# Kernel optimization log

Hardware: AMD Instinct MI355X
Metric: run time of the kernel (lower is better)

Reference implementation:

```python
import jax, jax.numpy as jnp
import numpy as np

B, D_IN, H1, H2, LAT, K = 32768, 512, 256, 128, 64, 2048
BN_EPS = 1e-5
COMMIT = 0.25


def _linear_w(k, i, o):
    # xavier-uniform-ish init
    lim = np.sqrt(6.0 / (i + o)).astype(np.float32)
    return jax.random.uniform(k, (i, o), jnp.float32, -lim, lim)


def _bn_params(keys, n):
    g = jax.random.uniform(keys[0], (n,), jnp.float32, 0.5, 1.5)
    b = 0.1 * jax.random.normal(keys[1], (n,), jnp.float32)
    m = 0.1 * jax.random.normal(keys[2], (n,), jnp.float32)
    v = jax.random.uniform(keys[3], (n,), jnp.float32, 0.5, 1.5)
    return g, b, m, v


def setup_inputs() -> dict:
    key = jax.random.key(0)
    ks = jax.random.split(key, 32)
    inp = {"x": jax.random.normal(ks[0], (B, D_IN), jnp.float32)}
    # encoder: 512 -> 256 -> 128 -> 64
    inp["ew1"], inp["eb1"] = _linear_w(ks[1], D_IN, H1), jnp.zeros((H1,), jnp.float32)
    inp["eg1"], inp["ebt1"], inp["em1"], inp["ev1"] = _bn_params(jax.random.split(ks[2], 4), H1)
    inp["ew2"], inp["eb2"] = _linear_w(ks[3], H1, H2), jnp.zeros((H2,), jnp.float32)
    inp["eg2"], inp["ebt2"], inp["em2"], inp["ev2"] = _bn_params(jax.random.split(ks[4], 4), H2)
    inp["ew3"], inp["eb3"] = _linear_w(ks[5], H2, LAT), jnp.zeros((LAT,), jnp.float32)
    # codebook (num_embeddings, latent_dim)
    inp["codebook"] = _linear_w(ks[6], K, LAT).reshape(K, LAT)
    # decoder: 64 -> 128 -> 256 -> 512
    inp["dw1"], inp["db1"] = _linear_w(ks[7], LAT, H2), jnp.zeros((H2,), jnp.float32)
    inp["dg1"], inp["dbt1"], inp["dm1"], inp["dv1"] = _bn_params(jax.random.split(ks[8], 4), H2)
    inp["dw2"], inp["db2"] = _linear_w(ks[9], H2, H1), jnp.zeros((H1,), jnp.float32)
    inp["dg2"], inp["dbt2"], inp["dm2"], inp["dv2"] = _bn_params(jax.random.split(ks[10], 4), H1)
    inp["dw3"], inp["db3"] = _linear_w(ks[11], H1, D_IN), jnp.zeros((D_IN,), jnp.float32)
    return inp


def _bn(x, g, b, m, v):
    # BatchNorm1d in eval mode: running stats
    return (x - m) * (g * jax.lax.rsqrt(v + BN_EPS)) + b


def reference(x, ew1, eb1, eg1, ebt1, em1, ev1,
              ew2, eb2, eg2, ebt2, em2, ev2,
              ew3, eb3, codebook,
              dw1, db1, dg1, dbt1, dm1, dv1,
              dw2, db2, dg2, dbt2, dm2, dv2,
              dw3, db3):
    # ---- encoder MLP (Dropout is identity in eval) ----
    h = _bn(jax.nn.relu(x @ ew1 + eb1), eg1, ebt1, em1, ev1)
    h = _bn(jax.nn.relu(h @ ew2 + eb2), eg2, ebt2, em2, ev2)
    z_e = h @ ew3 + eb3  # [B, LAT]

    # ---- vector quantization: cdist + argmin + gather ----
    # squared L2 distance (argmin-equivalent to cdist p=2)
    d2 = (jnp.sum(z_e * z_e, axis=1, keepdims=True)
          + jnp.sum(codebook * codebook, axis=1)[None, :]
          - 2.0 * (z_e @ codebook.T))  # [B, K]
    idx = jnp.argmin(d2, axis=-1)  # [B]
    z_q = codebook[idx]  # gather, [B, LAT]

    codebook_loss = jnp.mean((z_q - jax.lax.stop_gradient(z_e)) ** 2)
    commit_loss = jnp.mean((z_e - jax.lax.stop_gradient(z_q)) ** 2)
    vq_loss = codebook_loss + COMMIT * commit_loss

    # straight-through estimator
    z_q = z_e + jax.lax.stop_gradient(z_q - z_e)

    # ---- decoder MLP ----
    h = _bn(jax.nn.relu(z_q @ dw1 + db1), dg1, dbt1, dm1, dv1)
    h = _bn(jax.nn.relu(h @ dw2 + db2), dg2, dbt2, dm2, dv2)
    x_recon = h @ dw3 + db3  # [B, D_IN]

    recon_err = jnp.mean((x_recon - x) ** 2)
    return x_recon, vq_loss, idx, recon_err
```

## Files before the change

kernel.cpp:

```cpp
#include <hip/hip_runtime.h>

#define B_ROWS 32768
#define D_IN   512
#define H1_N   256
#define H2_N   128
#define LAT_N  64
#define K_CB   2048

#define BM 64
#define BN 128
#define BK 32

#define VQ_MARGIN 4.0e-3f

typedef __attribute__((ext_vector_type(8))) short s8v;
typedef __attribute__((ext_vector_type(4))) float f4v;

__device__ inline unsigned short f2bf(float f) {
    union { float f; unsigned u; } v; v.f = f;
    unsigned r = v.u + 0x7fffu + ((v.u >> 16) & 1u);
    return (unsigned short)(r >> 16);
}
__device__ inline float bf2f(unsigned short h) {
    union { unsigned u; float f; } v; v.u = ((unsigned)h) << 16;
    return v.f;
}

#define SWZ(row) ((((row) >> 2) & 7) << 3)

template <int MODE>
__global__ __launch_bounds__(256, 4) void gemm_fused(
    const float* __restrict__ A, const float* __restrict__ W,
    const float* __restrict__ bias,
    const float* __restrict__ bn_g, const float* __restrict__ bn_b,
    const float* __restrict__ bn_m, const float* __restrict__ bn_v,
    float* __restrict__ out, int M, int N)
{
    __shared__ float sA[BK][BM];
    __shared__ float sB[BK][BN];
    const int tid = threadIdx.x;
    const int tr = tid >> 4;
    const int tc = tid & 15;
    const int row0 = blockIdx.x * BM;
    const int n0   = blockIdx.y * BN;

    float acc[4][8];
#pragma unroll
    for (int i = 0; i < 4; ++i)
#pragma unroll
        for (int j = 0; j < 8; ++j) acc[i][j] = 0.f;

    for (int k0 = 0; k0 < M; k0 += BK) {
#pragma unroll
        for (int it = 0; it < 2; ++it) {
            int s = tid + it * 256;
            int m = s >> 3;
            int kq = s & 7;
            float4 v = *reinterpret_cast<const float4*>(
                &A[(size_t)(row0 + m) * M + k0 + kq * 4]);
            int kk = kq * 4;
            sA[kk + 0][m ^ SWZ(kk + 0)] = v.x;
            sA[kk + 1][m ^ SWZ(kk + 1)] = v.y;
            sA[kk + 2][m ^ SWZ(kk + 2)] = v.z;
            sA[kk + 3][m ^ SWZ(kk + 3)] = v.w;
        }
#pragma unroll
        for (int it = 0; it < 4; ++it) {
            int s = tid + it * 256;
            int k = s >> 5;
            int nq = s & 31;
            int n = n0 + nq * 4;
            float4 v = make_float4(0.f, 0.f, 0.f, 0.f);
            if (n < N)
                v = *reinterpret_cast<const float4*>(&W[(size_t)(k0 + k) * N + n]);
            *reinterpret_cast<float4*>(&sB[k][nq * 4]) = v;
        }
        __syncthreads();
#pragma unroll 4
        for (int k = 0; k < BK; ++k) {
            int ac = (tr * 4) ^ SWZ(k);
            float4 a0 = *reinterpret_cast<float4*>(&sA[k][ac]);
            float4 b0 = *reinterpret_cast<float4*>(&sB[k][tc * 8]);
            float4 b1 = *reinterpret_cast<float4*>(&sB[k][tc * 8 + 4]);
            float a[4] = {a0.x, a0.y, a0.z, a0.w};
            float b[8] = {b0.x, b0.y, b0.z, b0.w, b1.x, b1.y, b1.z, b1.w};
#pragma unroll
            for (int i = 0; i < 4; ++i)
#pragma unroll
                for (int j = 0; j < 8; ++j)
                    acc[i][j] = fmaf(a[i], b[j], acc[i][j]);
        }
        __syncthreads();
    }

    const int nb = n0 + tc * 8;
    if (nb < N) {
        float bi[8], sc[8], sh[8];
#pragma unroll
        for (int j = 0; j < 8; ++j) {
            int n = nb + j;
            bi[j] = bias[n];
            if (MODE == 0) {
                float s = bn_g[n] * rsqrtf(bn_v[n] + 1e-5f);
                sc[j] = s;
                sh[j] = bn_b[n] - bn_m[n] * s;
            }
        }
#pragma unroll
        for (int i = 0; i < 4; ++i) {
            int row = row0 + tr * 4 + i;
            float o[8];
#pragma unroll
            for (int j = 0; j < 8; ++j) {
                float v = acc[i][j] + bi[j];
                if (MODE == 0) {
                    v = v > 0.f ? v : 0.f;
                    v = v * sc[j] + sh[j];
                }
                o[j] = v;
            }
            *reinterpret_cast<float4*>(&out[(size_t)row * N + nb]) =
                make_float4(o[0], o[1], o[2], o[3]);
            *reinterpret_cast<float4*>(&out[(size_t)row * N + nb + 4]) =
                make_float4(o[4], o[5], o[6], o[7]);
        }
    }
}

__global__ __launch_bounds__(256) void wprep(
    const float* __restrict__ w, unsigned short* __restrict__ w_hi,
    unsigned short* __restrict__ w_lo, int K, int N)
{
    int idx = blockIdx.x * 256 + threadIdx.x;
    if (idx >= N * K) return;
    int n = idx / K, k = idx - n * K;
    float f = w[(size_t)k * N + n];
    unsigned u = __float_as_uint(f);
    float lo = f - __uint_as_float(u & 0xffff0000u);
    w_hi[idx] = (unsigned short)(u >> 16);
    w_lo[idx] = (unsigned short)(__float_as_uint(lo) >> 16);
}

template <int MODE, int K>
__global__ __launch_bounds__(256, 2) void mfma_gemm(
    const float* __restrict__ A,
    const unsigned short* __restrict__ w_hi,
    const unsigned short* __restrict__ w_lo,
    const float* __restrict__ bias,
    const float* __restrict__ bn_g, const float* __restrict__ bn_b,
    const float* __restrict__ bn_m, const float* __restrict__ bn_v,
    float* __restrict__ out,
    const float* __restrict__ xref, float* __restrict__ partials, int N)
{
    const int lane = threadIdx.x & 63;
    const int wv = threadIdx.x >> 6;
    const int wr = wv >> 1, wc = wv & 1;
    const int rbase = blockIdx.x * 128 + wr * 64;
    const int cbase = blockIdx.y * 128 + wc * 64;
    const int lr = lane & 15, lg = lane >> 4;

    f4v acc[4][4];
#pragma unroll
    for (int rt = 0; rt < 4; ++rt)
#pragma unroll
        for (int ct = 0; ct < 4; ++ct)
            acc[rt][ct] = (f4v){0.f, 0.f, 0.f, 0.f};

#pragma unroll
    for (int ks = 0; ks < K / 32; ++ks) {
        s8v ah[4], al[4], bh[4], bl[4];
#pragma unroll
        for (int rt = 0; rt < 4; ++rt) {
            const float* p =
                &A[(size_t)(rbase + rt * 16 + lr) * K + ks * 32 + lg * 8];
            float4 v0 = *reinterpret_cast<const float4*>(p);
            float4 v1 = *reinterpret_cast<const float4*>(p + 4);
            float fv[8] = {v0.x, v0.y, v0.z, v0.w, v1.x, v1.y, v1.z, v1.w};
            unsigned uu[8], ll[8];
#pragma unroll
            for (int j = 0; j < 8; ++j) {
                uu[j] = __float_as_uint(fv[j]);
                float lo = fv[j] - __uint_as_float(uu[j] & 0xffff0000u);
                ll[j] = __float_as_uint(lo);
            }
            union { s8v v; unsigned w[4]; } H, L;
#pragma unroll
            for (int m = 0; m < 4; ++m) {
                H.w[m] = __builtin_amdgcn_perm(uu[2 * m + 1], uu[2 * m], 0x07060302u);
                L.w[m] = __builtin_amdgcn_perm(ll[2 * m + 1], ll[2 * m], 0x07060302u);
            }
            ah[rt] = H.v;
            al[rt] = L.v;
        }
#pragma unroll
        for (int ct = 0; ct < 4; ++ct) {
            size_t off = (size_t)(cbase + ct * 16 + lr) * K + ks * 32 + lg * 8;
            bh[ct] = *reinterpret_cast<const s8v*>(&w_hi[off]);
            bl[ct] = *reinterpret_cast<const s8v*>(&w_lo[off]);
        }
#pragma unroll
        for (int rt = 0; rt < 4; ++rt)
#pragma unroll
            for (int ct = 0; ct < 4; ++ct) {
                acc[rt][ct] = __builtin_amdgcn_mfma_f32_16x16x32_bf16(
                    ah[rt], bh[ct], acc[rt][ct], 0, 0, 0);
                acc[rt][ct] = __builtin_amdgcn_mfma_f32_16x16x32_bf16(
                    al[rt], bh[ct], acc[rt][ct], 0, 0, 0);
                acc[rt][ct] = __builtin_amdgcn_mfma_f32_16x16x32_bf16(
                    ah[rt], bl[ct], acc[rt][ct], 0, 0, 0);
            }
    }

    float sq = 0.f;
#pragma unroll
    for (int ct = 0; ct < 4; ++ct) {
        int col = cbase + ct * 16 + lr;
        float bi = bias[col];
        float sc = 0.f, sh = 0.f;
        if (MODE == 0) {
            float s = bn_g[col] * rsqrtf(bn_v[col] + 1e-5f);
            sc = s;
            sh = bn_b[col] - bn_m[col] * s;
        }
#pragma unroll
        for (int rt = 0; rt < 4; ++rt)
#pragma unroll
            for (int i = 0; i < 4; ++i) {
                int row = rbase + rt * 16 + lg * 4 + i;
                float v = acc[rt][ct][i] + bi;
                if (MODE == 0) v = fmaxf(v, 0.f) * sc + sh;
                if (MODE == 2) {
                    float d = v - xref[(size_t)row * N + col];
                    sq = fmaf(d, d, sq);
                }
                out[(size_t)row * N + col] = v;
            }
    }
    if (MODE == 2) {
        __shared__ float red[256];
        red[threadIdx.x] = sq;
        __syncthreads();
        for (int off = 128; off > 0; off >>= 1) {
            if (threadIdx.x < off) red[threadIdx.x] += red[threadIdx.x + off];
            __syncthreads();
        }
        if (threadIdx.x == 0)
            partials[blockIdx.y * gridDim.x + blockIdx.x] = red[0];
    }
}

__global__ __launch_bounds__(256) void vq_prep(
    const float* __restrict__ cb, unsigned short* __restrict__ cb_hi,
    unsigned short* __restrict__ cb_lo, float* __restrict__ cn,
    int* __restrict__ rcnt)
{
    if (blockIdx.x == 0 && threadIdx.x == 0) rcnt[0] = 0;
    int j = blockIdx.x * 256 + threadIdx.x;
    float s = 0.f;
#pragma unroll
    for (int lq = 0; lq < 16; ++lq) {
        float4 v = *reinterpret_cast<const float4*>(&cb[(size_t)j * LAT_N + lq * 4]);
        float e[4] = {v.x, v.y, v.z, v.w};
        ushort4 h, l;
        unsigned short* hp = &h.x;
        unsigned short* lp = &l.x;
#pragma unroll
        for (int t = 0; t < 4; ++t) {
            s = fmaf(e[t], e[t], s);
            unsigned short hb = f2bf(e[t]);
            hp[t] = hb;
            lp[t] = f2bf(e[t] - bf2f(hb));
        }
        *reinterpret_cast<ushort4*>(&cb_hi[(size_t)j * LAT_N + lq * 4]) = h;
        *reinterpret_cast<ushort4*>(&cb_lo[(size_t)j * LAT_N + lq * 4]) = l;
    }
    cn[j] = s;
}

__global__ __launch_bounds__(256) void vq_mfma(
    const float* __restrict__ z, const unsigned short* __restrict__ cb_hi,
    const unsigned short* __restrict__ cb_lo, const float* __restrict__ cnorm,
    float4* __restrict__ cand)
{
    const int lane = threadIdx.x & 63;
    const int wid  = blockIdx.x * 4 + (threadIdx.x >> 6);
    const int rbase = (wid >> 3) * 64;
    const int cblk  = wid & 7;
    const int cbase = cblk * 256;
    const int lr = lane & 15;
    const int lg = lane >> 4;

    s8v a_hi[4][2], a_lo[4][2];
#pragma unroll
    for (int rt = 0; rt < 4; ++rt) {
        int row = rbase + rt * 16 + lr;
#pragma unroll
        for (int ks = 0; ks < 2; ++ks) {
            const float* p = &z[(size_t)row * LAT_N + ks * 32 + lg * 8];
            float4 v0 = *reinterpret_cast<const float4*>(p);
            float4 v1 = *reinterpret_cast<const float4*>(p + 4);
            float vv[8] = {v0.x, v0.y, v0.z, v0.w, v1.x, v1.y, v1.z, v1.w};
#pragma unroll
            for (int jj = 0; jj < 8; ++jj) {
                unsigned short hb = f2bf(vv[jj]);
                a_hi[rt][ks][jj] = (short)hb;
                a_lo[rt][ks][jj] = (short)f2bf(vv[jj] - bf2f(hb));
            }
        }
    }

    float b1[4][4], b2[4][4];
    int j1[4][4];
#pragma unroll
    for (int rt = 0; rt < 4; ++rt)
#pragma unroll
        for (int i = 0; i < 4; ++i) {
            b1[rt][i] = 3.4e38f; b2[rt][i] = 3.4e38f; j1[rt][i] = 0;
        }

    for (int ct = 0; ct < 16; ++ct) {
        int col = cbase + ct * 16 + lr;
        const unsigned short* ph = &cb_hi[(size_t)col * LAT_N + lg * 8];
        const unsigned short* pl = &cb_lo[(size_t)col * LAT_N + lg * 8];
        s8v bh0 = *reinterpret_cast<const s8v*>(ph);
        s8v bh1 = *reinterpret_cast<const s8v*>(ph + 32);
        s8v bl0 = *reinterpret_cast<const s8v*>(pl);
        s8v bl1 = *reinterpret_cast<const s8v*>(pl + 32);
        float cn = cnorm[col];
#pragma unroll
        for (int rt = 0; rt < 4; ++rt) {
            f4v acc = {0.f, 0.f, 0.f, 0.f};
            acc = __builtin_amdgcn_mfma_f32_16x16x32_bf16(a_hi[rt][0], bh0, acc, 0, 0, 0);
            acc = __builtin_amdgcn_mfma_f32_16x16x32_bf16(a_hi[rt][1], bh1, acc, 0, 0, 0);
            acc = __builtin_amdgcn_mfma_f32_16x16x32_bf16(a_lo[rt][0], bh0, acc, 0, 0, 0);
            acc = __builtin_amdgcn_mfma_f32_16x16x32_bf16(a_lo[rt][1], bh1, acc, 0, 0, 0);
            acc = __builtin_amdgcn_mfma_f32_16x16x32_bf16(a_hi[rt][0], bl0, acc, 0, 0, 0);
            acc = __builtin_amdgcn_mfma_f32_16x16x32_bf16(a_hi[rt][1], bl1, acc, 0, 0, 0);
#pragma unroll
            for (int i = 0; i < 4; ++i) {
                float d = fmaf(-2.f, acc[i], cn);
                if (d < b1[rt][i]) {
                    b2[rt][i] = b1[rt][i];
                    b1[rt][i] = d;
                    j1[rt][i] = col;
                } else if (d < b2[rt][i]) {
                    b2[rt][i] = d;
                }
            }
        }
    }

#pragma unroll
    for (int off = 1; off < 16; off <<= 1) {
#pragma unroll
        for (int rt = 0; rt < 4; ++rt)
#pragma unroll
            for (int i = 0; i < 4; ++i) {
                float o1 = __shfl_xor(b1[rt][i], off);
                float o2 = __shfl_xor(b2[rt][i], off);
                int oj = __shfl_xor(j1[rt][i], off);
                float nb2 = fminf(fmaxf(b1[rt][i], o1), fminf(b2[rt][i], o2));
                if (o1 < b1[rt][i] ||
                    (o1 == b1[rt][i] && oj < j1[rt][i])) {
                    b1[rt][i] = o1;
                    j1[rt][i] = oj;
                }
                b2[rt][i] = nb2;
            }
    }
    if (lr == 0) {
#pragma unroll
        for (int rt = 0; rt < 4; ++rt)
#pragma unroll
            for (int i = 0; i < 4; ++i) {
                int row = rbase + rt * 16 + lg * 4 + i;
                cand[(size_t)row * 8 + cblk] = make_float4(
                    b1[rt][i], __int_as_float(j1[rt][i]), b2[rt][i], 0.f);
            }
    }
}

__global__ __launch_bounds__(256) void vq_merge(
    const float4* __restrict__ cand, float* __restrict__ idxf,
    int* __restrict__ rlist, int* __restrict__ rcnt)
{
    int row = blockIdx.x * 256 + threadIdx.x;
    const float4* c = &cand[(size_t)row * 8];
    float4 c0 = c[0];
    float b1 = c0.x, b2 = c0.z;
    int j1 = __float_as_int(c0.y);
#pragma unroll
    for (int t = 1; t < 8; ++t) {
        float4 ct = c[t];
        float o1 = ct.x, o2 = ct.z;
        int oj = __float_as_int(ct.y);
        float nb2 = fminf(fmaxf(b1, o1), fminf(b2, o2));
        if (o1 < b1 || (o1 == b1 && oj < j1)) { b1 = o1; j1 = oj; }
        b2 = nb2;
    }
    idxf[row] = (float)j1;
    if (!(b2 - b1 >= VQ_MARGIN)) {
        int s = atomicAdd(rcnt, 1);
        if (s < B_ROWS) rlist[s] = row;
    }
}

#define RB 8
__global__ __launch_bounds__(256) void vq_repair(
    const int* __restrict__ rcnt, const int* __restrict__ rlist,
    const float* __restrict__ z, const float* __restrict__ cb,
    const float* __restrict__ cn, float* __restrict__ idxf)
{
    __shared__ float sz[RB][LAT_N];
    __shared__ float rv[256];
    __shared__ int ri[256];
    const int tid = threadIdx.x;
    const int count = min(rcnt[0], B_ROWS);
    if (blockIdx.x * RB >= count) return;
    for (int base = blockIdx.x * RB; base < count; base += gridDim.x * RB) {
        int nr = min(RB, count - base);
        __syncthreads();
        for (int s = tid; s < nr * LAT_N; s += 256) {
            int r = s >> 6, d = s & 63;
            int rr = rlist[base + r];
            rr = ((unsigned)rr < (unsigned)B_ROWS) ? rr : 0;
            sz[r][d] = z[(size_t)rr * LAT_N + d];
        }
        __syncthreads();
        float bv[RB];
        int bj[RB];
#pragma unroll
        for (int r = 0; r < RB; ++r) { bv[r] = 3.4e38f; bj[r] = 0; }
        for (int k = 0; k < K_CB / 256; ++k) {
            int cidx = tid + k * 256;
            float acc[RB];
#pragma unroll
            for (int r = 0; r < RB; ++r) acc[r] = 0.f;
            const float* cp = &cb[(size_t)cidx * LAT_N];
#pragma unroll 2
            for (int d4 = 0; d4 < 16; ++d4) {
                float4 cv = *reinterpret_cast<const float4*>(cp + d4 * 4);
#pragma unroll
                for (int r = 0; r < RB; ++r) {
                    acc[r] = fmaf(sz[r][d4 * 4 + 0], cv.x, acc[r]);
                    acc[r] = fmaf(sz[r][d4 * 4 + 1], cv.y, acc[r]);
                    acc[r] = fmaf(sz[r][d4 * 4 + 2], cv.z, acc[r]);
                    acc[r] = fmaf(sz[r][d4 * 4 + 3], cv.w, acc[r]);
                }
            }
            float cnv = cn[cidx];
#pragma unroll
            for (int r = 0; r < RB; ++r) {
                float d = fmaf(-2.f, acc[r], cnv);
                if (d < bv[r] || (d == bv[r] && cidx < bj[r])) {
                    bv[r] = d; bj[r] = cidx;
                }
            }
        }
        for (int r = 0; r < RB; ++r) {
            if (r >= nr) break;
            rv[tid] = bv[r];
            ri[tid] = bj[r];
            __syncthreads();
            for (int off = 128; off > 0; off >>= 1) {
                if (tid < off) {
                    float ov = rv[tid + off];
                    int oi = ri[tid + off];
                    if (ov < rv[tid] || (ov == rv[tid] && oi < ri[tid])) {
                        rv[tid] = ov; ri[tid] = oi;
                    }
                }
                __syncthreads();
            }
            if (tid == 0) {
                int rr = rlist[base + r];
                if ((unsigned)rr < (unsigned)B_ROWS)
                    idxf[rr] = (float)ri[0];
            }
            __syncthreads();
        }
    }
}

__global__ __launch_bounds__(256) void vq_zqloss(
    const float* __restrict__ idxf, const float* __restrict__ z,
    const float* __restrict__ cb, float* __restrict__ zq,
    float* __restrict__ partials)
{
    __shared__ float red[256];
    int tid = threadIdx.x;
    int row = blockIdx.x * 256 + tid;
    int bj = (int)idxf[row];
    bj = ((unsigned)bj < (unsigned)K_CB) ? bj : 0;
    float sq = 0.f;
#pragma unroll
    for (int lq = 0; lq < 16; ++lq) {
        float4 cv = *reinterpret_cast<const float4*>(&cb[(size_t)bj * LAT_N + lq * 4]);
        float4 zv = *reinterpret_cast<const float4*>(&z[(size_t)row * LAT_N + lq * 4]);
        *reinterpret_cast<float4*>(&zq[(size_t)row * LAT_N + lq * 4]) = cv;
        float d0 = cv.x - zv.x, d1 = cv.y - zv.y;
        float d2 = cv.z - zv.z, d3 = cv.w - zv.w;
        sq = fmaf(d0, d0, sq); sq = fmaf(d1, d1, sq);
        sq = fmaf(d2, d2, sq); sq = fmaf(d3, d3, sq);
    }
    red[tid] = sq;
    __syncthreads();
    for (int off = 128; off > 0; off >>= 1) {
        if (tid < off) red[tid] += red[tid + off];
        __syncthreads();
    }
    if (tid == 0) partials[blockIdx.x] = red[0];
}

__global__ __launch_bounds__(256) void finalize_kernel(
    const float* __restrict__ vqp, int nvq,
    const float* __restrict__ rep, int nre,
    float* __restrict__ vq_out, float* __restrict__ re_out)
{
    __shared__ float s[256];
    int tid = threadIdx.x;
    float a = 0.f;
    for (int i = tid; i < nvq; i += 256) a += vqp[i];
    s[tid] = a;
    __syncthreads();
    for (int off = 128; off > 0; off >>= 1) {
        if (tid < off) s[tid] += s[tid + off];
        __syncthreads();
    }
    if (tid == 0) *vq_out = 1.25f * s[0] / (float)(B_ROWS * LAT_N);
    __syncthreads();
    float b = 0.f;
    for (int i = tid; i < nre; i += 256) b += rep[i];
    s[tid] = b;
    __syncthreads();
    for (int off = 128; off > 0; off >>= 1) {
        if (tid < off) s[tid] += s[tid + off];
        __syncthreads();
    }
    if (tid == 0) *re_out = s[0] / (float)(B_ROWS * D_IN);
}

extern "C" void kernel_launch(void* const* d_in, const int* in_sizes, int n_in,
                              void* d_out, int out_size, void* d_ws, size_t ws_size,
                              hipStream_t stream)
{
    const float* x    = (const float*)d_in[0];
    const float* ew1  = (const float*)d_in[1];
    const float* eb1  = (const float*)d_in[2];
    const float* eg1  = (const float*)d_in[3];
    const float* ebt1 = (const float*)d_in[4];
    const float* em1  = (const float*)d_in[5];
    const float* ev1  = (const float*)d_in[6];
    const float* ew2  = (const float*)d_in[7];
    const float* eb2  = (const float*)d_in[8];
    const float* eg2  = (const float*)d_in[9];
    const float* ebt2 = (const float*)d_in[10];
    const float* em2  = (const float*)d_in[11];
    const float* ev2  = (const float*)d_in[12];
    const float* ew3  = (const float*)d_in[13];
    const float* eb3  = (const float*)d_in[14];
    const float* cb   = (const float*)d_in[15];
    const float* dw1  = (const float*)d_in[16];
    const float* db1  = (const float*)d_in[17];
    const float* dg1  = (const float*)d_in[18];
    const float* dbt1 = (const float*)d_in[19];
    const float* dm1  = (const float*)d_in[20];
    const float* dv1  = (const float*)d_in[21];
    const float* dw2  = (const float*)d_in[22];
    const float* db2  = (const float*)d_in[23];
    const float* dg2  = (const float*)d_in[24];
    const float* dbt2 = (const float*)d_in[25];
    const float* dm2  = (const float*)d_in[26];
    const float* dv2  = (const float*)d_in[27];
    const float* dw3  = (const float*)d_in[28];
    const float* db3  = (const float*)d_in[29];

    float* outf = (float*)d_out;
    const size_t XR_OFF = 0;
    const size_t VQ_OFF = (size_t)B_ROWS * D_IN;
    const size_t IDX_OFF = VQ_OFF + 1;
    const size_t RE_OFF = IDX_OFF + B_ROWS;

    float* wsf = (float*)d_ws;
    size_t off = 0;
    float* buf256 = wsf + off; off += (size_t)B_ROWS * H1_N;
    float* buf128 = wsf + off; off += (size_t)B_ROWS * H2_N;
    float* zbuf   = wsf + off; off += (size_t)B_ROWS * LAT_N;
    float* zqbuf  = wsf + off; off += (size_t)B_ROWS * LAT_N;
    float* cnbuf  = wsf + off; off += K_CB;
    float* vqp    = wsf + off; off += 128;
    float* rep    = wsf + off; off += 1024;
    unsigned short* cbhi = (unsigned short*)(wsf + off); off += K_CB * LAT_N / 2;
    unsigned short* cblo = (unsigned short*)(wsf + off); off += K_CB * LAT_N / 2;
    float4* candb = (float4*)(wsf + off); off += (size_t)B_ROWS * 8 * 4;
    int* rcnt  = (int*)(wsf + off); off += 16;
    int* rlist = (int*)(wsf + off); off += B_ROWS;
    unsigned short* w1hi = (unsigned short*)(wsf + off); off += (H2_N * LAT_N) / 2;
    unsigned short* w1lo = (unsigned short*)(wsf + off); off += (H2_N * LAT_N) / 2;
    unsigned short* w2hi = (unsigned short*)(wsf + off); off += (H1_N * H2_N) / 2;
    unsigned short* w2lo = (unsigned short*)(wsf + off); off += (H1_N * H2_N) / 2;
    unsigned short* w3hi = (unsigned short*)(wsf + off); off += (D_IN * H1_N) / 2;
    unsigned short* w3lo = (unsigned short*)(wsf + off); off += (D_IN * H1_N) / 2;

    dim3 blk(256);
    const int GX = B_ROWS / BM;
    const int GXM = B_ROWS / 128;

    vq_prep<<<dim3(K_CB / 256), blk, 0, stream>>>(cb, cbhi, cblo, cnbuf, rcnt);
    wprep<<<dim3((LAT_N * H2_N + 255) / 256), blk, 0, stream>>>(dw1, w1hi, w1lo, LAT_N, H2_N);
    wprep<<<dim3((H2_N * H1_N + 255) / 256), blk, 0, stream>>>(dw2, w2hi, w2lo, H2_N, H1_N);
    wprep<<<dim3((H1_N * D_IN + 255) / 256), blk, 0, stream>>>(dw3, w3hi, w3lo, H1_N, D_IN);

    gemm_fused<0><<<dim3(GX, H1_N / BN), blk, 0, stream>>>(
        x, ew1, eb1, eg1, ebt1, em1, ev1, buf256, D_IN, H1_N);
    gemm_fused<0><<<dim3(GX, 1), blk, 0, stream>>>(
        buf256, ew2, eb2, eg2, ebt2, em2, ev2, buf128, H1_N, H2_N);
    gemm_fused<1><<<dim3(GX, 1), blk, 0, stream>>>(
        buf128, ew3, eb3, nullptr, nullptr, nullptr, nullptr, zbuf, H2_N, LAT_N);

    vq_mfma<<<dim3(1024), blk, 0, stream>>>(zbuf, cbhi, cblo, cnbuf, candb);
    vq_merge<<<dim3(B_ROWS / 256), blk, 0, stream>>>(
        candb, outf + IDX_OFF, rlist, rcnt);
    vq_repair<<<dim3(256), blk, 0, stream>>>(
        rcnt, rlist, zbuf, cb, cnbuf, outf + IDX_OFF);
    vq_zqloss<<<dim3(B_ROWS / 256), blk, 0, stream>>>(
        outf + IDX_OFF, zbuf, cb, zqbuf, vqp);

    mfma_gemm<0, LAT_N><<<dim3(GXM, H2_N / 128), blk, 0, stream>>>(
        zqbuf, w1hi, w1lo, db1, dg1, dbt1, dm1, dv1, buf128, nullptr, nullptr, H2_N);
    mfma_gemm<0, H2_N><<<dim3(GXM, H1_N / 128), blk, 0, stream>>>(
        buf128, w2hi, w2lo, db2, dg2, dbt2, dm2, dv2, buf256, nullptr, nullptr, H1_N);
    mfma_gemm<2, H1_N><<<dim3(GXM, D_IN / 128), blk, 0, stream>>>(
        buf256, w3hi, w3lo, db3, nullptr, nullptr, nullptr, nullptr,
        outf + XR_OFF, x, rep, D_IN);

    finalize_kernel<<<dim3(1), blk, 0, stream>>>(
        vqp, 128, rep, 1024, outf + VQ_OFF, outf + RE_OFF);
}
```

Baseline: 417.9 us.

## Store decoder activations as split bf16 hi/lo and retile encoder GEMMs

Decoder MFMA GEMMs now read activations already split into bf16 hi/lo planes, written by the previous layer's epilogue and by vq_zqloss (which copies the pre-split codebook rows). This removes the per-load fp32-to-bf16 split work in the GEMM inner loop while keeping the same number of bytes per activation. The encoder SIMT GEMM gains a 128-row tile variant for the first layer, with changed column mapping and occupancy hints. The lo part now uses round-to-nearest, which slightly changes the numerics. The epilogue issues scalar 16-bit stores to two planes, which may coalesce poorly.

```diff
diff --git a/kernel.cpp b/kernel.cpp
--- a/kernel.cpp
+++ b/kernel.cpp
@@ -7,7 +7,6 @@
 #define LAT_N  64
 #define K_CB   2048
 
-#define BM 64
 #define BN 128
 #define BK 32
 
@@ -28,31 +27,32 @@
 
 #define SWZ(row) ((((row) >> 2) & 7) << 3)
 
-template <int MODE>
-__global__ __launch_bounds__(256, 4) void gemm_fused(
+template <int MODE, int BMT>
+__global__ __launch_bounds__(256, (BMT == 128) ? 2 : 6) void gemm_fused(
     const float* __restrict__ A, const float* __restrict__ W,
     const float* __restrict__ bias,
     const float* __restrict__ bn_g, const float* __restrict__ bn_b,
     const float* __restrict__ bn_m, const float* __restrict__ bn_v,
     float* __restrict__ out, int M, int N)
 {
-    __shared__ float sA[BK][BM];
+    constexpr int MR = BMT / 16;
+    __shared__ float sA[BK][BMT];
     __shared__ float sB[BK][BN];
     const int tid = threadIdx.x;
     const int tr = tid >> 4;
     const int tc = tid & 15;
-    const int row0 = blockIdx.x * BM;
+    const int row0 = blockIdx.x * BMT;
     const int n0   = blockIdx.y * BN;
 
-    float acc[4][8];
-#pragma unroll
-    for (int i = 0; i < 4; ++i)
+    float acc[MR][8];
+#pragma unroll
+    for (int i = 0; i < MR; ++i)
 #pragma unroll
         for (int j = 0; j < 8; ++j) acc[i][j] = 0.f;
 
     for (int k0 = 0; k0 < M; k0 += BK) {
 #pragma unroll
-        for (int it = 0; it < 2; ++it) {
+        for (int it = 0; it < BMT / 32; ++it) {
             int s = tid + it * 256;
             int m = s >> 3;
             int kq = s & 7;
@@ -78,14 +78,21 @@
         __syncthreads();
 #pragma unroll 4
         for (int k = 0; k < BK; ++k) {
-            int ac = (tr * 4) ^ SWZ(k);
-            float4 a0 = *reinterpret_cast<float4*>(&sA[k][ac]);
-            float4 b0 = *reinterpret_cast<float4*>(&sB[k][tc * 8]);
-            float4 b1 = *reinterpret_cast<float4*>(&sB[k][tc * 8 + 4]);
-            float a[4] = {a0.x, a0.y, a0.z, a0.w};
+            int ac = (tr * MR) ^ SWZ(k);
+            float a[MR];
+            {
+                float4 a0 = *reinterpret_cast<float4*>(&sA[k][ac]);
+                a[0] = a0.x; a[1] = a0.y; a[2] = a0.z; a[3] = a0.w;
+                if constexpr (MR == 8) {
+                    float4 a1 = *reinterpret_cast<float4*>(&sA[k][ac + 4]);
+                    a[4] = a1.x; a[5] = a1.y; a[6] = a1.z; a[7] = a1.w;
+                }
+            }
+            float4 b0 = *reinterpret_cast<float4*>(&sB[k][tc * 4]);
+            float4 b1 = *reinterpret_cast<float4*>(&sB[k][64 + tc * 4]);
             float b[8] = {b0.x, b0.y, b0.z, b0.w, b1.x, b1.y, b1.z, b1.w};
 #pragma unroll
-            for (int i = 0; i < 4; ++i)
+            for (int i = 0; i < MR; ++i)
 #pragma unroll
                 for (int j = 0; j < 8; ++j)
                     acc[i][j] = fmaf(a[i], b[j], acc[i][j]);
@@ -93,36 +100,45 @@
         __syncthreads();
     }
 
-    const int nb = n0 + tc * 8;
-    if (nb < N) {
-        float bi[8], sc[8], sh[8];
-#pragma unroll
-        for (int j = 0; j < 8; ++j) {
-            int n = nb + j;
-            bi[j] = bias[n];
-            if (MODE == 0) {
-                float s = bn_g[n] * rsqrtf(bn_v[n] + 1e-5f);
-                sc[j] = s;
-                sh[j] = bn_b[n] - bn_m[n] * s;
-            }
-        }
-#pragma unroll
-        for (int i = 0; i < 4; ++i) {
-            int row = row0 + tr * 4 + i;
-            float o[8];
-#pragma unroll
-            for (int j = 0; j < 8; ++j) {
-                float v = acc[i][j] + bi[j];
+    const int nb0 = n0 + tc * 4;
+    const int nb1 = n0 + 64 + tc * 4;
+    float bi[8], sc[8], sh[8];
+#pragma unroll
+    for (int g = 0; g < 2; ++g) {
+        int nb = g ? nb1 : nb0;
+        if (nb < N) {
+#pragma unroll
+            for (int j = 0; j < 4; ++j) {
+                int n = nb + j;
+                bi[g * 4 + j] = bias[n];
                 if (MODE == 0) {
-                    v = v > 0.f ? v : 0.f;
-                    v = v * sc[j] + sh[j];
-                }
-                o[j] = v;
-            }
-            *reinterpret_cast<float4*>(&out[(size_t)row * N + nb]) =
-                make_float4(o[0], o[1], o[2], o[3]);
-            *reinterpret_cast<float4*>(&out[(size_t)row * N + nb + 4]) =
-                make_float4(o[4], o[5], o[6], o[7]);
+                    float s = bn_g[n] * rsqrtf(bn_v[n] + 1e-5f);
+                    sc[g * 4 + j] = s;
+                    sh[g * 4 + j] = bn_b[n] - bn_m[n] * s;
+                }
+            }
+        }
+    }
+#pragma unroll
+    for (int i = 0; i < MR; ++i) {
+        int row = row0 + tr * MR + i;
+#pragma unroll
+        for (int g = 0; g < 2; ++g) {
+            int nb = g ? nb1 : nb0;
+            if (nb < N) {
+                float o[4];
+#pragma unroll
+                for (int j = 0; j < 4; ++j) {
+                    float v = acc[i][g * 4 + j] + bi[g * 4 + j];
+                    if (MODE == 0) {
+                        v = v > 0.f ? v : 0.f;
+                        v = v * sc[g * 4 + j] + sh[g * 4 + j];
+                    }
+                    o[j] = v;
+                }
+                *reinterpret_cast<float4*>(&out[(size_t)row * N + nb]) =
+                    make_float4(o[0], o[1], o[2], o[3]);
+            }
         }
     }
 }
@@ -138,18 +154,20 @@
     unsigned u = __float_as_uint(f);
     float lo = f - __uint_as_float(u & 0xffff0000u);
     w_hi[idx] = (unsigned short)(u >> 16);
-    w_lo[idx] = (unsigned short)(__float_as_uint(lo) >> 16);
+    w_lo[idx] = f2bf(lo);
 }
 
 template <int MODE, int K>
 __global__ __launch_bounds__(256, 2) void mfma_gemm(
-    const float* __restrict__ A,
+    const unsigned short* __restrict__ A_hi,
+    const unsigned short* __restrict__ A_lo,
     const unsigned short* __restrict__ w_hi,
     const unsigned short* __restrict__ w_lo,
     const float* __restrict__ bias,
     const float* __restrict__ bn_g, const float* __restrict__ bn_b,
     const float* __restrict__ bn_m, const float* __restrict__ bn_v,
-    float* __restrict__ out,
+    unsigned short* __restrict__ out_hi, unsigned short* __restrict__ out_lo,
+    float* __restrict__ out_f32,
     const float* __restrict__ xref, float* __restrict__ partials, int N)
 {
     const int lane = threadIdx.x & 63;
@@ -171,26 +189,9 @@
         s8v ah[4], al[4], bh[4], bl[4];
 #pragma unroll
         for (int rt = 0; rt < 4; ++rt) {
-            const float* p =
-                &A[(size_t)(rbase + rt * 16 + lr) * K + ks * 32 + lg * 8];
-            float4 v0 = *reinterpret_cast<const float4*>(p);
-            float4 v1 = *reinterpret_cast<const float4*>(p + 4);
-            float fv[8] = {v0.x, v0.y, v0.z, v0.w, v1.x, v1.y, v1.z, v1.w};
-            unsigned uu[8], ll[8];
-#pragma unroll
-            for (int j = 0; j < 8; ++j) {
-                uu[j] = __float_as_uint(fv[j]);
-                float lo = fv[j] - __uint_as_float(uu[j] & 0xffff0000u);
-                ll[j] = __float_as_uint(lo);
-            }
-            union { s8v v; unsigned w[4]; } H, L;
-#pragma unroll
-            for (int m = 0; m < 4; ++m) {
-                H.w[m] = __builtin_amdgcn_perm(uu[2 * m + 1], uu[2 * m], 0x07060302u);
-                L.w[m] = __builtin_amdgcn_perm(ll[2 * m + 1], ll[2 * m], 0x07060302u);
-            }
-            ah[rt] = H.v;
-            al[rt] = L.v;
+            size_t off = (size_t)(rbase + rt * 16 + lr) * K + ks * 32 + lg * 8;
+            ah[rt] = *reinterpret_cast<const s8v*>(&A_hi[off]);
+            al[rt] = *reinterpret_cast<const s8v*>(&A_lo[off]);
         }
 #pragma unroll
         for (int ct = 0; ct < 4; ++ct) {
@@ -228,12 +229,18 @@
             for (int i = 0; i < 4; ++i) {
                 int row = rbase + rt * 16 + lg * 4 + i;
                 float v = acc[rt][ct][i] + bi;
-                if (MODE == 0) v = fmaxf(v, 0.f) * sc + sh;
+                if (MODE == 0) {
+                    v = fmaxf(v, 0.f) * sc + sh;
+                    unsigned u = __float_as_uint(v);
+                    out_hi[(size_t)row * N + col] = (unsigned short)(u >> 16);
+                    out_lo[(size_t)row * N + col] =
+                        f2bf(v - __uint_as_float(u & 0xffff0000u));
+                }
                 if (MODE == 2) {
                     float d = v - xref[(size_t)row * N + col];
                     sq = fmaf(d, d, sq);
-                }
-                out[(size_t)row * N + col] = v;
+                    out_f32[(size_t)row * N + col] = v;
+                }
             }
     }
     if (MODE == 2) {
@@ -484,7 +491,10 @@
 
 __global__ __launch_bounds__(256) void vq_zqloss(
     const float* __restrict__ idxf, const float* __restrict__ z,
-    const float* __restrict__ cb, float* __restrict__ zq,
+    const float* __restrict__ cb,
+    const unsigned short* __restrict__ cbhi,
+    const unsigned short* __restrict__ cblo,
+    unsigned short* __restrict__ zqhi, unsigned short* __restrict__ zqlo,
     float* __restrict__ partials)
 {
     __shared__ float red[256];
@@ -497,12 +507,18 @@
     for (int lq = 0; lq < 16; ++lq) {
         float4 cv = *reinterpret_cast<const float4*>(&cb[(size_t)bj * LAT_N + lq * 4]);
         float4 zv = *reinterpret_cast<const float4*>(&z[(size_t)row * LAT_N + lq * 4]);
-        *reinterpret_cast<float4*>(&zq[(size_t)row * LAT_N + lq * 4]) = cv;
         float d0 = cv.x - zv.x, d1 = cv.y - zv.y;
         float d2 = cv.z - zv.z, d3 = cv.w - zv.w;
         sq = fmaf(d0, d0, sq); sq = fmaf(d1, d1, sq);
         sq = fmaf(d2, d2, sq); sq = fmaf(d3, d3, sq);
     }
+    const uint4* gh = reinterpret_cast<const uint4*>(&cbhi[(size_t)bj * LAT_N]);
+    const uint4* gl = reinterpret_cast<const uint4*>(&cblo[(size_t)bj * LAT_N]);
+    uint4* dh = reinterpret_cast<uint4*>(&zqhi[(size_t)row * LAT_N]);
+    uint4* dl = reinterpret_cast<uint4*>(&zqlo[(size_t)row * LAT_N]);
+#pragma unroll
+    for (int q = 0; q < 8; ++q) { dh[q] = gh[q]; dl[q] = gl[q]; }
+
     red[tid] = sq;
     __syncthreads();
     for (int off = 128; off > 0; off >>= 1) {
@@ -586,7 +602,6 @@
     float* buf256 = wsf + off; off += (size_t)B_ROWS * H1_N;
     float* buf128 = wsf + off; off += (size_t)B_ROWS * H2_N;
     float* zbuf   = wsf + off; off += (size_t)B_ROWS * LAT_N;
-    float* zqbuf  = wsf + off; off += (size_t)B_ROWS * LAT_N;
     float* cnbuf  = wsf + off; off += K_CB;
     float* vqp    = wsf + off; off += 128;
     float* rep    = wsf + off; off += 1024;
@@ -601,21 +616,26 @@
     unsigned short* w2lo = (unsigned short*)(wsf + off); off += (H1_N * H2_N) / 2;
     unsigned short* w3hi = (unsigned short*)(wsf + off); off += (D_IN * H1_N) / 2;
     unsigned short* w3lo = (unsigned short*)(wsf + off); off += (D_IN * H1_N) / 2;
+    unsigned short* zqhi = (unsigned short*)(wsf + off); off += (size_t)B_ROWS * LAT_N / 2;
+    unsigned short* zqlo = (unsigned short*)(wsf + off); off += (size_t)B_ROWS * LAT_N / 2;
+
+    unsigned short* h1hi = (unsigned short*)buf128;
+    unsigned short* h1lo = (unsigned short*)(buf128 + (size_t)B_ROWS * 64);
+    unsigned short* h2hi = (unsigned short*)buf256;
+    unsigned short* h2lo = (unsigned short*)(buf256 + (size_t)B_ROWS * 128);
 
     dim3 blk(256);
-    const int GX = B_ROWS / BM;
-    const int GXM = B_ROWS / 128;
 
     vq_prep<<<dim3(K_CB / 256), blk, 0, stream>>>(cb, cbhi, cblo, cnbuf, rcnt);
     wprep<<<dim3((LAT_N * H2_N + 255) / 256), blk, 0, stream>>>(dw1, w1hi, w1lo, LAT_N, H2_N);
     wprep<<<dim3((H2_N * H1_N + 255) / 256), blk, 0, stream>>>(dw2, w2hi, w2lo, H2_N, H1_N);
     wprep<<<dim3((H1_N * D_IN + 255) / 256), blk, 0, stream>>>(dw3, w3hi, w3lo, H1_N, D_IN);
 
-    gemm_fused<0><<<dim3(GX, H1_N / BN), blk, 0, stream>>>(
+    gemm_fused<0, 128><<<dim3(B_ROWS / 128, H1_N / BN), blk, 0, stream>>>(
         x, ew1, eb1, eg1, ebt1, em1, ev1, buf256, D_IN, H1_N);
-    gemm_fused<0><<<dim3(GX, 1), blk, 0, stream>>>(
+    gemm_fused<0, 64><<<dim3(B_ROWS / 64, 1), blk, 0, stream>>>(
         buf256, ew2, eb2, eg2, ebt2, em2, ev2, buf128, H1_N, H2_N);
-    gemm_fused<1><<<dim3(GX, 1), blk, 0, stream>>>(
+    gemm_fused<1, 64><<<dim3(B_ROWS / 64, 1), blk, 0, stream>>>(
         buf128, ew3, eb3, nullptr, nullptr, nullptr, nullptr, zbuf, H2_N, LAT_N);
 
     vq_mfma<<<dim3(1024), blk, 0, stream>>>(zbuf, cbhi, cblo, cnbuf, candb);
@@ -624,15 +644,17 @@
     vq_repair<<<dim3(256), blk, 0, stream>>>(
         rcnt, rlist, zbuf, cb, cnbuf, outf + IDX_OFF);
     vq_zqloss<<<dim3(B_ROWS / 256), blk, 0, stream>>>(
-        outf + IDX_OFF, zbuf, cb, zqbuf, vqp);
-
-    mfma_gemm<0, LAT_N><<<dim3(GXM, H2_N / 128), blk, 0, stream>>>(
-        zqbuf, w1hi, w1lo, db1, dg1, dbt1, dm1, dv1, buf128, nullptr, nullptr, H2_N);
-    mfma_gemm<0, H2_N><<<dim3(GXM, H1_N / 128), blk, 0, stream>>>(
-        buf128, w2hi, w2lo, db2, dg2, dbt2, dm2, dv2, buf256, nullptr, nullptr, H1_N);
-    mfma_gemm<2, H1_N><<<dim3(GXM, D_IN / 128), blk, 0, stream>>>(
-        buf256, w3hi, w3lo, db3, nullptr, nullptr, nullptr, nullptr,
-        outf + XR_OFF, x, rep, D_IN);
+        outf + IDX_OFF, zbuf, cb, cbhi, cblo, zqhi, zqlo, vqp);
+
+    mfma_gemm<0, LAT_N><<<dim3(B_ROWS / 128, H2_N / 128), blk, 0, stream>>>(
+        zqhi, zqlo, w1hi, w1lo, db1, dg1, dbt1, dm1, dv1,
+        h1hi, h1lo, nullptr, nullptr, nullptr, H2_N);
+    mfma_gemm<0, H2_N><<<dim3(B_ROWS / 128, H1_N / 128), blk, 0, stream>>>(
+        h1hi, h1lo, w2hi, w2lo, db2, dg2, dbt2, dm2, dv2,
+        h2hi, h2lo, nullptr, nullptr, nullptr, H1_N);
+    mfma_gemm<2, H1_N><<<dim3(B_ROWS / 128, D_IN / 128), blk, 0, stream>>>(
+        h2hi, h2lo, w3hi, w3lo, db3, nullptr, nullptr, nullptr, nullptr,
+        nullptr, nullptr, outf + XR_OFF, x, rep, D_IN);
 
     finalize_kernel<<<dim3(1), blk, 0, stream>>>(
         vqp, 128, rep, 1024, outf + VQ_OFF, outf + RE_OFF);
```

New measurement: 417.8 us. Within noise of the previous version (-0.0%).
